# Kernel tuning notes

Measured on AMD Instinct MI355X. Metric: run time of the kernel, lower is better.

Reference implementation:

```python
import jax, jax.numpy as jnp
import numpy as np

N = 40000          # spots (nodes)
G = 3000           # genes (input features)
C = 20             # num_classes
E = N * 16         # edges (avg degree 16)


def _uniform(key, shape, stdv):
    return jax.random.uniform(key, shape, jnp.float32, -stdv, stdv)


def _linear_params(key, n_in, n_out):
    # torch Linear default init: U(-1/sqrt(in), 1/sqrt(in)); stored as [in, out]
    k1, k2 = jax.random.split(key)
    s = 1.0 / np.sqrt(n_in)
    return _uniform(k1, (n_in, n_out), s), _uniform(k2, (n_out,), s)


def setup_inputs() -> dict:
    key = jax.random.key(0)
    ks = jax.random.split(key, 32)
    x = jax.random.normal(ks[0], (N, G), jnp.float32)
    adj_rows = jax.random.randint(ks[1], (E,), 0, N, jnp.int32)
    adj_cols = jax.random.randint(ks[2], (E,), 0, N, jnp.int32)
    adj_vals = jax.random.uniform(ks[3], (E,), jnp.float32)

    # GCN weights: GraphConvolution init U(-1/sqrt(out), 1/sqrt(out)), no bias
    def gcn_w(k, fi, fo):
        return _uniform(k, (fi, fo), 1.0 / np.sqrt(fo))

    inp = {
        "x": x, "adj_rows": adj_rows, "adj_cols": adj_cols, "adj_vals": adj_vals,
        "W1": gcn_w(ks[4], G, 512), "W2": gcn_w(ks[5], 512, 256),
        "W3": gcn_w(ks[6], 256, 128), "W4": gcn_w(ks[7], 128, 128),
        "W5": gcn_w(ks[8], 128, C),
    }
    # AE linear layers
    for name, (fi, fo), k in [
        ("enc1", (G, 512), ks[9]), ("enc2", (512, 256), ks[10]),
        ("enc3", (256, 128), ks[11]), ("zl", (128, 128), ks[12]),
        ("dec1", (128, 128), ks[13]), ("dec2", (128, 256), ks[14]),
        ("dec3", (256, 512), ks[15]), ("xbar", (512, G), ks[16]),
    ]:
        w, b = _linear_params(k, fi, fo)
        inp[name + "_w"], inp[name + "_b"] = w, b
    # Attention projection vectors (Linear(in_size, 1, bias=False))
    inp["a1"] = _uniform(ks[17], (512,), 1.0 / np.sqrt(512))
    inp["a2"] = _uniform(ks[18], (256,), 1.0 / np.sqrt(256))
    inp["a3"] = _uniform(ks[19], (128,), 1.0 / np.sqrt(128))
    inp["a4"] = _uniform(ks[20], (128,), 1.0 / np.sqrt(128))
    inp["scale"] = jax.random.normal(ks[21], (G,), jnp.float32)
    inp["additive"] = jax.random.normal(ks[22], (G,), jnp.float32)
    return inp


def _spmm(rows, cols, vals, dense, n):
    # out[r] = sum_e vals[e] * dense[cols[e]] for rows[e]==r  (sparse [n,n] @ dense)
    return jax.ops.segment_sum(vals[:, None] * dense[cols], rows, num_segments=n)


def _gcn(x, rows, cols, vals, W, n, active=True):
    out = _spmm(rows, cols, vals, x @ W, n)
    return jax.nn.relu(out) if active else out


def _attn(h, t, a):
    # stack two [N,D] branches, softmax over the branch axis, weighted sum
    z = jnp.stack([h, t], axis=1)           # [N,2,D]
    w = jnp.einsum('nbd,d->nb', z, a)        # [N,2]
    beta = jax.nn.softmax(w, axis=1)
    return jnp.einsum('nb,nbd->nd', beta, z)


def reference(x, adj_rows, adj_cols, adj_vals,
              W1, W2, W3, W4, W5,
              enc1_w, enc1_b, enc2_w, enc2_b, enc3_w, enc3_b, zl_w, zl_b,
              dec1_w, dec1_b, dec2_w, dec2_b, dec3_w, dec3_b, xbar_w, xbar_b,
              a1, a2, a3, a4, scale, additive):
    n = x.shape[0]
    # autoencoder
    t1 = jax.nn.relu(x @ enc1_w + enc1_b)
    t2 = jax.nn.relu(t1 @ enc2_w + enc2_b)
    t3 = jax.nn.relu(t2 @ enc3_w + enc3_b)
    z = t3 @ zl_w + zl_b
    d1 = jax.nn.relu(z @ dec1_w + dec1_b)
    d2 = jax.nn.relu(d1 @ dec2_w + dec2_b)
    d3 = jax.nn.relu(d2 @ dec3_w + dec3_b)
    x_bar = d3 @ xbar_w + xbar_b
    # GCN stack with attention-fused AE skip connections
    h = _gcn(x, adj_rows, adj_cols, adj_vals, W1, n)
    emb = _attn(h, t1, a1)
    h = _gcn(emb, adj_rows, adj_cols, adj_vals, W2, n)
    emb = _attn(h, t2, a2)
    h = _gcn(emb, adj_rows, adj_cols, adj_vals, W3, n)
    emb = _attn(h, t3, a3)
    h = _gcn(emb, adj_rows, adj_cols, adj_vals, W4, n)
    emb = _attn(h, z, a4)
    output = _gcn(emb, adj_rows, adj_cols, adj_vals, W5, n, active=False)
    return output, x_bar, jax.nn.sigmoid(scale), jnp.exp(additive)
```

## Files before the change

### kernel.cpp

```cpp
#include <hip/hip_runtime.h>
#include <cmath>

typedef unsigned short u16;
typedef unsigned int u32;
typedef __attribute__((ext_vector_type(8))) short short8;
typedef __attribute__((ext_vector_type(4))) short short4v;
typedef __attribute__((ext_vector_type(4))) float f32x4;

__device__ __forceinline__ float bf2f(u16 h) {
  union { u32 u; float f; } v; v.u = ((u32)h) << 16; return v.f;
}
__device__ __forceinline__ u16 f2bf(float f) {
  union { float f; u32 u; } v; v.f = f;
  u32 u = v.u;
  u32 r = (u + 0x7FFFu + ((u >> 16) & 1u)) >> 16;
  return (u16)r;
}

__global__ void convx_kernel(const float* __restrict__ x, u16* __restrict__ A0) {
  int idx = blockIdx.x * 256 + threadIdx.x;
  int r = blockIdx.y;
  if (idx >= 752) return;
  short4v o;
  if (r < 40000 && idx < 750) {
    float4 v = *(const float4*)(x + (size_t)r * 3000 + idx * 4);
    o[0] = (short)f2bf(v.x); o[1] = (short)f2bf(v.y);
    o[2] = (short)f2bf(v.z); o[3] = (short)f2bf(v.w);
  } else {
    o[0] = 0; o[1] = 0; o[2] = 0; o[3] = 0;
  }
  *(short4v*)(A0 + (size_t)r * 3008 + idx * 4) = o;
}

__global__ void convw_kernel(const float* __restrict__ W, u16* __restrict__ Wt,
                             int K, int N, int Kp) {
  int k = blockIdx.x * 256 + threadIdx.x;
  int n = blockIdx.y;
  if (k >= Kp) return;
  float v = (k < K && n < N) ? W[(size_t)k * N + n] : 0.f;
  Wt[(size_t)n * Kp + k] = f2bf(v);
}

__global__ void zero_kernel(int* p, int n) {
  int i = blockIdx.x * 256 + threadIdx.x;
  if (i < n) p[i] = 0;
}
__global__ void count_kernel(const int* __restrict__ rows, int* __restrict__ counts, int E) {
  int i = blockIdx.x * 256 + threadIdx.x;
  if (i < E) atomicAdd(&counts[rows[i]], 1);
}
__global__ __launch_bounds__(1024) void scan_kernel(const int* __restrict__ counts,
                                                    int* __restrict__ rowptr,
                                                    int* __restrict__ cursor, int n) {
  __shared__ int buf[1024];
  __shared__ int carry_s;
  int tid = threadIdx.x;
  if (tid == 0) carry_s = 0;
  __syncthreads();
  for (int base = 0; base < n; base += 1024) {
    int i = base + tid;
    int v = (i < n) ? counts[i] : 0;
    buf[tid] = v;
    __syncthreads();
    for (int off = 1; off < 1024; off <<= 1) {
      int tv = (tid >= off) ? buf[tid - off] : 0;
      __syncthreads();
      buf[tid] += tv;
      __syncthreads();
    }
    int incl = buf[tid];
    int carry = carry_s;
    if (i < n) { int ex = carry + incl - v; rowptr[i] = ex; cursor[i] = ex; }
    __syncthreads();
    if (tid == 1023) carry_s = carry + incl;
    __syncthreads();
  }
  if (tid == 0) rowptr[n] = carry_s;
}
__global__ void scatter_kernel(const int* __restrict__ rows, const int* __restrict__ cols,
                               const float* __restrict__ vals, int* __restrict__ cursor,
                               int* __restrict__ cols_s, float* __restrict__ vals_s, int E) {
  int i = blockIdx.x * 256 + threadIdx.x;
  if (i < E) {
    int r = rows[i];
    int p = atomicAdd(&cursor[r], 1);
    cols_s[p] = cols[i];
    vals_s[p] = vals[i];
  }
}

#define BM 128
#define BN 128
#define BK 32

template <bool BIAS, bool RELU, bool OUTBF16, int CH>
__global__ __launch_bounds__(256, 2) void gemm_bf16(
    const u16* __restrict__ A, int lda, const u16* __restrict__ Bt, int ldb,
    void* __restrict__ C1, int ldc,
    const float* __restrict__ bias, int M, int Nreal, int K, int MT, int NT) {
  __shared__ __align__(16) u16 As[2][BM * BK];
  __shared__ __align__(16) u16 Bs[2][BN * BK];
  const int lin = blockIdx.x;
  const int per = CH * NT;
  const int g = lin / per;
  const int r0 = lin - g * per;
  const int bx0 = g * CH;
  const int cw = min(CH, MT - bx0);
  const int bx = bx0 + r0 % cw;
  const int by = r0 / cw;

  const int tid = threadIdx.x;
  const int lane = tid & 63;
  const int wave = tid >> 6;
  const int mblk = bx * BM;
  const int nblk = by * BN;
  const int wm = (wave & 1) * 64;
  const int wn = (wave >> 1) * 64;
  const int ml = lane & 15;
  const int kg = lane >> 4;

  f32x4 acc[4][4];
#pragma unroll
  for (int i = 0; i < 4; ++i)
#pragma unroll
    for (int j = 0; j < 4; ++j) acc[i][j] = (f32x4)(0.f);

  const int nk = K / BK;
  const int sr = tid >> 2;
  const int sc = (tid & 3) * 8;
  const u16* gA0 = A + (size_t)(mblk + sr) * lda + sc;
  const u16* gA1 = A + (size_t)(mblk + sr + 64) * lda + sc;
  const u16* gB0 = Bt + (size_t)(nblk + sr) * ldb + sc;
  const u16* gB1 = Bt + (size_t)(nblk + sr + 64) * ldb + sc;

  auto stage = [&](int buf, int kt) {
    const int ko = kt * BK;
    u16* lA = &As[buf][0] + wave * 512;
    u16* lB = &Bs[buf][0] + wave * 512;
    __builtin_amdgcn_global_load_lds((const void*)(gA0 + ko), (void*)lA, 16, 0, 0);
    __builtin_amdgcn_global_load_lds((const void*)(gA1 + ko), (void*)(lA + 2048), 16, 0, 0);
    __builtin_amdgcn_global_load_lds((const void*)(gB0 + ko), (void*)lB, 16, 0, 0);
    __builtin_amdgcn_global_load_lds((const void*)(gB1 + ko), (void*)(lB + 2048), 16, 0, 0);
  };

  stage(0, 0);
  asm volatile("s_waitcnt vmcnt(0)" ::: "memory");
  __syncthreads();

  int cur = 0;
  for (int kt = 0; kt < nk; ++kt) {
    if (kt + 1 < nk) stage(cur ^ 1, kt + 1);
    short8 af[4], bfr[4];
#pragma unroll
    for (int i = 0; i < 4; ++i) {
      af[i] = *(const short8*)&As[cur][(wm + i * 16 + ml) * BK + kg * 8];
      bfr[i] = *(const short8*)&Bs[cur][(wn + i * 16 + ml) * BK + kg * 8];
    }
#pragma unroll
    for (int i = 0; i < 4; ++i)
#pragma unroll
      for (int j = 0; j < 4; ++j)
        acc[i][j] = __builtin_amdgcn_mfma_f32_16x16x32_bf16(af[i], bfr[j], acc[i][j], 0, 0, 0);
    asm volatile("s_waitcnt vmcnt(0)" ::: "memory");
    __syncthreads();
    cur ^= 1;
  }

#pragma unroll
  for (int i = 0; i < 4; ++i) {
    const int row0 = mblk + wm + i * 16 + kg * 4;
#pragma unroll
    for (int j = 0; j < 4; ++j) {
      const int col = nblk + wn + j * 16 + ml;
      if (col < Nreal) {
        float bv = BIAS ? bias[col] : 0.f;
#pragma unroll
        for (int r = 0; r < 4; ++r) {
          const int row = row0 + r;
          if (row < M) {
            float v = acc[i][j][r] + bv;
            if (RELU) v = fmaxf(v, 0.f);
            if (OUTBF16)
              ((u16*)C1)[(size_t)row * ldc + col] = f2bf(v);
            else
              ((float*)C1)[(size_t)row * ldc + col] = v;
          }
        }
      }
    }
  }
}

template <bool BIAS, bool RELU, bool OUTBF16, bool SPLIT>
__global__ __launch_bounds__(512, 1) void gemm256(
    const u16* __restrict__ A, int lda, const u16* __restrict__ Bt, int ldb,
    void* __restrict__ C1, void* __restrict__ C2, int ldc,
    const float* __restrict__ bias, int M, int Nreal, int K, int MT2, int NT) {
  __shared__ __align__(16) u16 lds[2][2][256 * 64];
  const int tid = threadIdx.x;
  const int lane = tid & 63;
  const int wave = tid >> 6;
  const int wm = wave >> 2;
  const int wn = wave & 3;
  const int ml = lane & 15;
  const int kg = lane >> 4;

  const int grp = blockIdx.x / (8 * NT);
  const int rr = blockIdx.x % (8 * NT);
  const int nb = min(8, MT2 - grp * 8);
  const int bx = grp * 8 + rr % nb;
  const int by = rr / nb;
  const int mblk = bx * 256;
  const int nblk = by * 256;

  f32x4 acc[8][4];
#pragma unroll
  for (int i = 0; i < 8; ++i)
#pragma unroll
    for (int j = 0; j < 4; ++j) acc[i][j] = (f32x4)(0.f);

  const int srow = tid >> 3;
  const int clog = (tid & 7) ^ (srow & 7);
  const size_t abase = (size_t)(mblk + srow) * lda + clog * 8;
  const size_t bbase = (size_t)(nblk + srow) * ldb + clog * 8;
  const int NKT = K / 64;

  auto stageA = [&](int d, int kt, int h) {
    u16* dst = &lds[d][0][0] + h * 4096 + wave * 512;
    const u16* src = A + abase + (size_t)h * 64 * lda + kt * 64;
    __builtin_amdgcn_global_load_lds((const void*)src, (void*)dst, 16, 0, 0);
  };
  auto stageB = [&](int d, int kt, int h) {
    u16* dst = &lds[d][1][0] + h * 4096 + wave * 512;
    const u16* src = Bt + bbase + (size_t)h * 64 * ldb + kt * 64;
    __builtin_amdgcn_global_load_lds((const void*)src, (void*)dst, 16, 0, 0);
  };
  auto stageAll = [&](int d, int kt) {
    stageB(d, kt, 0); stageB(d, kt, 1); stageB(d, kt, 2); stageB(d, kt, 3);
    stageA(d, kt, 0); stageA(d, kt, 1); stageA(d, kt, 2); stageA(d, kt, 3);
  };
  auto readA = [&](int d, int im, int kk) -> short8 {
    const int r = wm * 128 + im * 16 + ml;
    const int ch = (kk * 4 + kg) ^ (r & 7);
    return *(const short8*)&lds[d][0][r * 64 + ch * 8];
  };
  auto readB = [&](int d, int j, int kk) -> short8 {
    const int r = wn * 64 + j * 16 + ml;
    const int ch = (kk * 4 + kg) ^ (r & 7);
    return *(const short8*)&lds[d][1][r * 64 + ch * 8];
  };

  stageAll(0, 0);
  __syncthreads();

  for (int kt = 0; kt < NKT; ++kt) {
    const int d = kt & 1;
    if (kt + 1 < NKT) stageAll(d ^ 1, kt + 1);

    short8 b[4][2];
#pragma unroll
    for (int j = 0; j < 4; ++j) { b[j][0] = readB(d, j, 0); b[j][1] = readB(d, j, 1); }
    short8 aC0k0 = readA(d, 0, 0), aC0k1 = readA(d, 0, 1);
    short8 aC1k0 = readA(d, 1, 0), aC1k1 = readA(d, 1, 1);
#pragma unroll
    for (int q = 0; q < 4; ++q) {
      short8 aN0k0, aN0k1, aN1k0, aN1k1;
      if (q < 3) {
        aN0k0 = readA(d, 2 * (q + 1), 0);     aN0k1 = readA(d, 2 * (q + 1), 1);
        aN1k0 = readA(d, 2 * (q + 1) + 1, 0); aN1k1 = readA(d, 2 * (q + 1) + 1, 1);
      }
      __builtin_amdgcn_s_setprio(1);
#pragma unroll
      for (int j = 0; j < 4; ++j) {
        acc[2 * q][j]     = __builtin_amdgcn_mfma_f32_16x16x32_bf16(aC0k0, b[j][0], acc[2 * q][j], 0, 0, 0);
        acc[2 * q + 1][j] = __builtin_amdgcn_mfma_f32_16x16x32_bf16(aC1k0, b[j][0], acc[2 * q + 1][j], 0, 0, 0);
      }
#pragma unroll
      for (int j = 0; j < 4; ++j) {
        acc[2 * q][j]     = __builtin_amdgcn_mfma_f32_16x16x32_bf16(aC0k1, b[j][1], acc[2 * q][j], 0, 0, 0);
        acc[2 * q + 1][j] = __builtin_amdgcn_mfma_f32_16x16x32_bf16(aC1k1, b[j][1], acc[2 * q + 1][j], 0, 0, 0);
      }
      __builtin_amdgcn_s_setprio(0);
      if (q < 3) { aC0k0 = aN0k0; aC0k1 = aN0k1; aC1k0 = aN1k0; aC1k1 = aN1k1; }
    }
    __syncthreads();
  }

  const int crow0 = mblk + wm * 128;
  const int ccol0 = nblk + wn * 64;
#pragma unroll
  for (int i = 0; i < 8; ++i) {
    const int row0 = crow0 + i * 16 + kg * 4;
#pragma unroll
    for (int j = 0; j < 4; ++j) {
      const int col = ccol0 + j * 16 + ml;
      if (SPLIT) {
        const bool second = (nblk >= 512);
        const float bv = second ? 0.f : bias[col];
#pragma unroll
        for (int r = 0; r < 4; ++r) {
          const int row = row0 + r;
          if (row < M) {
            float v = acc[i][j][r] + bv;
            if (!second) v = fmaxf(v, 0.f);
            u16* dst = second ? (u16*)C2 : (u16*)C1;
            dst[(size_t)row * 512 + (second ? col - 512 : col)] = f2bf(v);
          }
        }
      } else if (col < Nreal) {
        const float bv = BIAS ? bias[col] : 0.f;
#pragma unroll
        for (int r = 0; r < 4; ++r) {
          const int row = row0 + r;
          if (row < M) {
            float v = acc[i][j][r] + bv;
            if (RELU) v = fmaxf(v, 0.f);
            if (OUTBF16)
              ((u16*)C1)[(size_t)row * ldc + col] = f2bf(v);
            else
              ((float*)C1)[(size_t)row * ldc + col] = v;
          }
        }
      }
    }
  }
}

template <int D, bool RELU>
__global__ __launch_bounds__(256) void spmm_vec(const int* __restrict__ rowptr,
                                                const int* __restrict__ colidx,
                                                const float* __restrict__ vals,
                                                const u16* __restrict__ X,
                                                u16* __restrict__ Y) {
  constexpr int VE = D / 64;
  const int wave = threadIdx.x >> 6, lane = threadIdx.x & 63;
  const int row = blockIdx.x * 4 + wave;
  const int co = lane * VE;
  float acc[VE];
#pragma unroll
  for (int j = 0; j < VE; ++j) acc[j] = 0.f;
  const int s = rowptr[row], e = rowptr[row + 1];
  for (int i = s; i < e; ++i) {
    const int c = colidx[i];
    const float v = vals[i];
    const u16* xr = X + (size_t)c * D + co;
    if constexpr (VE == 8) {
      short8 x8 = *(const short8*)xr;
#pragma unroll
      for (int j = 0; j < 8; ++j) acc[j] += v * bf2f((u16)x8[j]);
    } else if constexpr (VE == 4) {
      short4v x4 = *(const short4v*)xr;
#pragma unroll
      for (int j = 0; j < 4; ++j) acc[j] += v * bf2f((u16)x4[j]);
    } else {
      u32 x2 = *(const u32*)xr;
      acc[0] += v * bf2f((u16)(x2 & 0xffffu));
      acc[1] += v * bf2f((u16)(x2 >> 16));
    }
  }
  u16* yr = Y + (size_t)row * D + co;
  if constexpr (VE == 8) {
    short8 o;
#pragma unroll
    for (int j = 0; j < 8; ++j) { float f = RELU ? fmaxf(acc[j], 0.f) : acc[j]; o[j] = (short)f2bf(f); }
    *(short8*)yr = o;
  } else if constexpr (VE == 4) {
    short4v o;
#pragma unroll
    for (int j = 0; j < 4; ++j) { float f = RELU ? fmaxf(acc[j], 0.f) : acc[j]; o[j] = (short)f2bf(f); }
    *(short4v*)yr = o;
  } else {
    float f0 = RELU ? fmaxf(acc[0], 0.f) : acc[0];
    float f1 = RELU ? fmaxf(acc[1], 0.f) : acc[1];
    *(u32*)yr = (u32)f2bf(f0) | ((u32)f2bf(f1) << 16);
  }
}

__global__ __launch_bounds__(64) void spmm_out_kernel(const int* __restrict__ rowptr,
                                                      const int* __restrict__ colidx,
                                                      const float* __restrict__ vals,
                                                      const u16* __restrict__ X,
                                                      float* __restrict__ Y) {
  int row = blockIdx.x;
  int c = threadIdx.x;
  float acc = 0.f;
  int s = rowptr[row], e = rowptr[row + 1];
  for (int i = s; i < e; ++i) {
    int col = colidx[i];
    float v = vals[i];
    if (c < 20) acc += v * bf2f(X[(size_t)col * 20 + c]);
  }
  if (c < 20) Y[(size_t)row * 20 + c] = acc;
}

template <int D>
__global__ __launch_bounds__(256) void attn_vec(const u16* __restrict__ h,
                                                const u16* __restrict__ t,
                                                const float* __restrict__ a,
                                                u16* __restrict__ emb) {
  constexpr int VE = D / 64;
  const int wave = threadIdx.x >> 6, lane = threadIdx.x & 63;
  const int row = blockIdx.x * 4 + wave;
  const int co = lane * VE;
  const u16* hr = h + (size_t)row * D + co;
  const u16* tr = t + (size_t)row * D + co;
  float hv[VE], tv[VE];
  if constexpr (VE == 8) {
    short8 h8 = *(const short8*)hr, t8 = *(const short8*)tr;
#pragma unroll
    for (int j = 0; j < 8; ++j) { hv[j] = bf2f((u16)h8[j]); tv[j] = bf2f((u16)t8[j]); }
  } else if constexpr (VE == 4) {
    short4v h4 = *(const short4v*)hr, t4 = *(const short4v*)tr;
#pragma unroll
    for (int j = 0; j < 4; ++j) { hv[j] = bf2f((u16)h4[j]); tv[j] = bf2f((u16)t4[j]); }
  } else {
    u32 h2 = *(const u32*)hr, t2 = *(const u32*)tr;
    hv[0] = bf2f((u16)(h2 & 0xffffu)); hv[1] = bf2f((u16)(h2 >> 16));
    tv[0] = bf2f((u16)(t2 & 0xffffu)); tv[1] = bf2f((u16)(t2 >> 16));
  }
  float wh = 0.f, wt = 0.f;
#pragma unroll
  for (int j = 0; j < VE; ++j) {
    float av = a[co + j];
    wh += av * hv[j];
    wt += av * tv[j];
  }
  for (int off = 32; off; off >>= 1) {
    wh += __shfl_xor(wh, off);
    wt += __shfl_xor(wt, off);
  }
  float m = fmaxf(wh, wt);
  float e1 = expf(wh - m), e2 = expf(wt - m);
  float inv = 1.f / (e1 + e2);
  float b1 = e1 * inv, b2 = e2 * inv;
  u16* er = emb + (size_t)row * D + co;
  if constexpr (VE == 8) {
    short8 o;
#pragma unroll
    for (int j = 0; j < 8; ++j) o[j] = (short)f2bf(b1 * hv[j] + b2 * tv[j]);
    *(short8*)er = o;
  } else if constexpr (VE == 4) {
    short4v o;
#pragma unroll
    for (int j = 0; j < 4; ++j) o[j] = (short)f2bf(b1 * hv[j] + b2 * tv[j]);
    *(short4v*)er = o;
  } else {
    *(u32*)er = (u32)f2bf(b1 * hv[0] + b2 * tv[0]) | ((u32)f2bf(b1 * hv[1] + b2 * tv[1]) << 16);
  }
}

__global__ __launch_bounds__(64) void xw5_kernel(const u16* __restrict__ emb,
                                                 const float* __restrict__ W5,
                                                 u16* __restrict__ xw5) {
  int row = blockIdx.x;
  int c = threadIdx.x;
  if (c >= 20) return;
  const short8* er = (const short8*)(emb + (size_t)row * 128);
  float acc = 0.f;
#pragma unroll
  for (int k8 = 0; k8 < 16; ++k8) {
    short8 v = er[k8];
#pragma unroll
    for (int j = 0; j < 8; ++j) acc += bf2f((u16)v[j]) * W5[(k8 * 8 + j) * 20 + c];
  }
  xw5[(size_t)row * 20 + c] = f2bf(acc);
}

__global__ void sig_exp_kernel(const float* __restrict__ scale, const float* __restrict__ additive,
                               float* __restrict__ osig, float* __restrict__ oexp, int g) {
  int i = blockIdx.x * 256 + threadIdx.x;
  if (i < g) {
    osig[i] = 1.f / (1.f + expf(-scale[i]));
    oexp[i] = expf(additive[i]);
  }
}

extern "C" void kernel_launch(void* const* d_in, const int* in_sizes, int n_in,
                              void* d_out, int out_size, void* d_ws, size_t ws_size,
                              hipStream_t stream) {
  (void)n_in; (void)out_size; (void)ws_size;
  const float* x      = (const float*)d_in[0];
  const int*   arows  = (const int*)d_in[1];
  const int*   acols  = (const int*)d_in[2];
  const float* avals  = (const float*)d_in[3];
  const float* W1     = (const float*)d_in[4];
  const float* W2     = (const float*)d_in[5];
  const float* W3     = (const float*)d_in[6];
  const float* W4     = (const float*)d_in[7];
  const float* W5     = (const float*)d_in[8];
  const float* enc1_w = (const float*)d_in[9],  *enc1_b = (const float*)d_in[10];
  const float* enc2_w = (const float*)d_in[11], *enc2_b = (const float*)d_in[12];
  const float* enc3_w = (const float*)d_in[13], *enc3_b = (const float*)d_in[14];
  const float* zl_w   = (const float*)d_in[15], *zl_b   = (const float*)d_in[16];
  const float* dec1_w = (const float*)d_in[17], *dec1_b = (const float*)d_in[18];
  const float* dec2_w = (const float*)d_in[19], *dec2_b = (const float*)d_in[20];
  const float* dec3_w = (const float*)d_in[21], *dec3_b = (const float*)d_in[22];
  const float* xbar_w = (const float*)d_in[23], *xbar_b = (const float*)d_in[24];
  const float* a1 = (const float*)d_in[25], *a2 = (const float*)d_in[26];
  const float* a3 = (const float*)d_in[27], *a4 = (const float*)d_in[28];
  const float* scale = (const float*)d_in[29], *additive = (const float*)d_in[30];

  const int E = in_sizes[1];
  const int N = 40000, G = 3000, Kx = 3008;
  const int Mp = 40192;

  float* out      = (float*)d_out;
  float* out_gcn  = out;
  float* out_xbar = out + (size_t)N * 20;
  float* out_sig  = out_xbar + (size_t)N * G;
  float* out_exp  = out_sig + G;

  char* wsb = (char*)d_ws;
  size_t off = 0;
  auto alloc = [&](size_t b) -> void* {
    void* p = wsb + off;
    off = (off + b + 255) & ~(size_t)255;
    return p;
  };
  u16* A0    = (u16*)alloc((size_t)Mp * Kx * 2);
  u16* t1    = (u16*)alloc((size_t)Mp * 512 * 2);
  u16* t2    = (u16*)alloc((size_t)Mp * 256 * 2);
  u16* t3    = (u16*)alloc((size_t)Mp * 128 * 2);
  u16* zb    = (u16*)alloc((size_t)Mp * 128 * 2);
  u16* dd1   = (u16*)alloc((size_t)Mp * 128 * 2);
  u16* dd2   = (u16*)alloc((size_t)Mp * 256 * 2);
  u16* dd3   = (u16*)alloc((size_t)Mp * 512 * 2);
  u16* xw    = (u16*)alloc((size_t)Mp * 512 * 2);
  u16* hb    = (u16*)alloc((size_t)Mp * 512 * 2);
  u16* emb   = (u16*)alloc((size_t)Mp * 512 * 2);
  u16* xw5   = (u16*)alloc((size_t)N * 20 * 2);
  u16* catT  = (u16*)alloc((size_t)1024 * Kx * 2);
  u16* enc2T = (u16*)alloc((size_t)256 * 512 * 2);
  u16* enc3T = (u16*)alloc((size_t)128 * 256 * 2);
  u16* zlT   = (u16*)alloc((size_t)128 * 128 * 2);
  u16* dec1T = (u16*)alloc((size_t)128 * 128 * 2);
  u16* dec2T = (u16*)alloc((size_t)256 * 128 * 2);
  u16* dec3T = (u16*)alloc((size_t)512 * 256 * 2);
  u16* xbarT = (u16*)alloc((size_t)3072 * 512 * 2);
  u16* W2T   = (u16*)alloc((size_t)256 * 512 * 2);
  u16* W3T   = (u16*)alloc((size_t)128 * 256 * 2);
  u16* W4T   = (u16*)alloc((size_t)128 * 128 * 2);
  int* counts = (int*)alloc((size_t)N * 4);
  int* rowptr = (int*)alloc((size_t)(N + 1) * 4);
  int* cursor = (int*)alloc((size_t)N * 4);
  int* colss  = (int*)alloc((size_t)E * 4);
  float* valss = (float*)alloc((size_t)E * 4);

  convx_kernel<<<dim3(3, Mp), 256, 0, stream>>>(x, A0);
  auto convw = [&](const float* W, u16* Wt, int K, int Nw, int Kp, int Np) {
    convw_kernel<<<dim3((Kp + 255) / 256, Np), 256, 0, stream>>>(W, Wt, K, Nw, Kp);
  };
  convw(enc1_w, catT,             3000, 512, Kx, 512);
  convw(W1,     catT + 512 * Kx,  3000, 512, Kx, 512);
  convw(enc2_w, enc2T, 512, 256, 512, 256);
  convw(enc3_w, enc3T, 256, 128, 256, 128);
  convw(zl_w,   zlT,   128, 128, 128, 128);
  convw(dec1_w, dec1T, 128, 128, 128, 128);
  convw(dec2_w, dec2T, 128, 256, 128, 256);
  convw(dec3_w, dec3T, 256, 512, 256, 512);
  convw(xbar_w, xbarT, 512, 3000, 512, 3072);
  convw(W2,     W2T,   512, 256, 512, 256);
  convw(W3,     W3T,   256, 128, 256, 128);
  convw(W4,     W4T,   128, 128, 128, 128);

  zero_kernel<<<(N + 255) / 256, 256, 0, stream>>>(counts, N);
  count_kernel<<<(E + 255) / 256, 256, 0, stream>>>(arows, counts, E);
  scan_kernel<<<1, 1024, 0, stream>>>(counts, rowptr, cursor, N);
  scatter_kernel<<<(E + 255) / 256, 256, 0, stream>>>(arows, acols, avals, cursor, colss, valss, E);

  const int MT = 313;
  const int MT2 = 157;
  gemm256<false, false, true, true><<<MT2 * 4, 512, 0, stream>>>(
      A0, Kx, catT, Kx, t1, xw, 512, enc1_b, N, 1024, Kx, MT2, 4);
  gemm_bf16<true, true, true, 32><<<MT * 2, 256, 0, stream>>>(
      t1, 512, enc2T, 512, t2, 256, enc2_b, N, 256, 512, MT, 2);
  gemm_bf16<true, true, true, 32><<<MT * 1, 256, 0, stream>>>(
      t2, 256, enc3T, 256, t3, 128, enc3_b, N, 128, 256, MT, 1);
  gemm_bf16<true, false, true, 32><<<MT * 1, 256, 0, stream>>>(
      t3, 128, zlT, 128, zb, 128, zl_b, N, 128, 128, MT, 1);
  gemm_bf16<true, true, true, 32><<<MT * 1, 256, 0, stream>>>(
      zb, 128, dec1T, 128, dd1, 128, dec1_b, N, 128, 128, MT, 1);
  gemm_bf16<true, true, true, 32><<<MT * 2, 256, 0, stream>>>(
      dd1, 128, dec2T, 128, dd2, 256, dec2_b, N, 256, 128, MT, 2);
  gemm256<true, true, true, false><<<MT2 * 2, 512, 0, stream>>>(
      dd2, 256, dec3T, 256, dd3, nullptr, 512, dec3_b, N, 512, 256, MT2, 2);
  gemm256<true, false, false, false><<<MT2 * 12, 512, 0, stream>>>(
      dd3, 512, xbarT, 512, out_xbar, nullptr, 3000, xbar_b, N, 3000, 512, MT2, 12);

  spmm_vec<512, true><<<N / 4, 256, 0, stream>>>(rowptr, colss, valss, xw, hb);
  attn_vec<512><<<N / 4, 256, 0, stream>>>(hb, t1, a1, emb);
  gemm_bf16<false, false, true, 32><<<MT * 2, 256, 0, stream>>>(
      emb, 512, W2T, 512, xw, 256, nullptr, N, 256, 512, MT, 2);
  spmm_vec<256, true><<<N / 4, 256, 0, stream>>>(rowptr, colss, valss, xw, hb);
  attn_vec<256><<<N / 4, 256, 0, stream>>>(hb, t2, a2, emb);
  gemm_bf16<false, false, true, 32><<<MT * 1, 256, 0, stream>>>(
      emb, 256, W3T, 256, xw, 128, nullptr, N, 128, 256, MT, 1);
  spmm_vec<128, true><<<N / 4, 256, 0, stream>>>(rowptr, colss, valss, xw, hb);
  attn_vec<128><<<N / 4, 256, 0, stream>>>(hb, t3, a3, emb);
  gemm_bf16<false, false, true, 32><<<MT * 1, 256, 0, stream>>>(
      emb, 128, W4T, 128, xw, 128, nullptr, N, 128, 128, MT, 1);
  spmm_vec<128, true><<<N / 4, 256, 0, stream>>>(rowptr, colss, valss, xw, hb);
  attn_vec<128><<<N / 4, 256, 0, stream>>>(hb, zb, a4, emb);

  xw5_kernel<<<N, 64, 0, stream>>>(emb, W5, xw5);
  spmm_out_kernel<<<N, 64, 0, stream>>>(rowptr, colss, valss, xw5, out_gcn);

  sig_exp_kernel<<<(G + 255) / 256, 256, 0, stream>>>(scale, additive, out_sig, out_exp, G);
}
```

Measured before the change: 1.472 ms.

## Fuse SpMM with attention and shrink big GEMM tiles to 128x256

Merges each SpMM with the attention combine that follows it, so the aggregated features stay in registers and the hb intermediate is never written or read back from global memory. The large GEMM kernel now uses 128-row M tiles instead of 256, which doubles the grid and cuts per-block LDS and accumulator registers. The dec3 GEMM moves from the 256-tile kernel to the smaller gemm_bf16 kernel. Smaller tiles raise occupancy and improve load balance over the CUs, but they lower per-block reuse of the B operand.

```diff
diff --git a/kernel.cpp b/kernel.cpp
--- a/kernel.cpp
+++ b/kernel.cpp
@@ -192,11 +192,12 @@
 }
 
 template <bool BIAS, bool RELU, bool OUTBF16, bool SPLIT>
-__global__ __launch_bounds__(512, 1) void gemm256(
+__global__ __launch_bounds__(512, 1) void gemm256v2(
     const u16* __restrict__ A, int lda, const u16* __restrict__ Bt, int ldb,
     void* __restrict__ C1, void* __restrict__ C2, int ldc,
-    const float* __restrict__ bias, int M, int Nreal, int K, int MT2, int NT) {
-  __shared__ __align__(16) u16 lds[2][2][256 * 64];
+    const float* __restrict__ bias, int M, int Nreal, int K, int MT, int NT) {
+  __shared__ __align__(16) u16 As[2][128 * 64];
+  __shared__ __align__(16) u16 Bs[2][256 * 64];
   const int tid = threadIdx.x;
   const int lane = tid & 63;
   const int wave = tid >> 6;
@@ -207,15 +208,15 @@
 
   const int grp = blockIdx.x / (8 * NT);
   const int rr = blockIdx.x % (8 * NT);
-  const int nb = min(8, MT2 - grp * 8);
+  const int nb = min(8, MT - grp * 8);
   const int bx = grp * 8 + rr % nb;
   const int by = rr / nb;
-  const int mblk = bx * 256;
+  const int mblk = bx * 128;
   const int nblk = by * 256;
 
-  f32x4 acc[8][4];
-#pragma unroll
-  for (int i = 0; i < 8; ++i)
+  f32x4 acc[4][4];
+#pragma unroll
+  for (int i = 0; i < 4; ++i)
 #pragma unroll
     for (int j = 0; j < 4; ++j) acc[i][j] = (f32x4)(0.f);
 
@@ -226,28 +227,28 @@
   const int NKT = K / 64;
 
   auto stageA = [&](int d, int kt, int h) {
-    u16* dst = &lds[d][0][0] + h * 4096 + wave * 512;
+    u16* dst = &As[d][0] + h * 4096 + wave * 512;
     const u16* src = A + abase + (size_t)h * 64 * lda + kt * 64;
     __builtin_amdgcn_global_load_lds((const void*)src, (void*)dst, 16, 0, 0);
   };
   auto stageB = [&](int d, int kt, int h) {
-    u16* dst = &lds[d][1][0] + h * 4096 + wave * 512;
+    u16* dst = &Bs[d][0] + h * 4096 + wave * 512;
     const u16* src = Bt + bbase + (size_t)h * 64 * ldb + kt * 64;
     __builtin_amdgcn_global_load_lds((const void*)src, (void*)dst, 16, 0, 0);
   };
   auto stageAll = [&](int d, int kt) {
     stageB(d, kt, 0); stageB(d, kt, 1); stageB(d, kt, 2); stageB(d, kt, 3);
-    stageA(d, kt, 0); stageA(d, kt, 1); stageA(d, kt, 2); stageA(d, kt, 3);
+    stageA(d, kt, 0); stageA(d, kt, 1);
   };
   auto readA = [&](int d, int im, int kk) -> short8 {
-    const int r = wm * 128 + im * 16 + ml;
+    const int r = wm * 64 + im * 16 + ml;
     const int ch = (kk * 4 + kg) ^ (r & 7);
-    return *(const short8*)&lds[d][0][r * 64 + ch * 8];
+    return *(const short8*)&As[d][r * 64 + ch * 8];
   };
   auto readB = [&](int d, int j, int kk) -> short8 {
     const int r = wn * 64 + j * 16 + ml;
     const int ch = (kk * 4 + kg) ^ (r & 7);
-    return *(const short8*)&lds[d][1][r * 64 + ch * 8];
+    return *(const short8*)&Bs[d][r * 64 + ch * 8];
   };
 
   stageAll(0, 0);
@@ -263,11 +264,11 @@
     short8 aC0k0 = readA(d, 0, 0), aC0k1 = readA(d, 0, 1);
     short8 aC1k0 = readA(d, 1, 0), aC1k1 = readA(d, 1, 1);
 #pragma unroll
-    for (int q = 0; q < 4; ++q) {
+    for (int q = 0; q < 2; ++q) {
       short8 aN0k0, aN0k1, aN1k0, aN1k1;
-      if (q < 3) {
-        aN0k0 = readA(d, 2 * (q + 1), 0);     aN0k1 = readA(d, 2 * (q + 1), 1);
-        aN1k0 = readA(d, 2 * (q + 1) + 1, 0); aN1k1 = readA(d, 2 * (q + 1) + 1, 1);
+      if (q == 0) {
+        aN0k0 = readA(d, 2, 0); aN0k1 = readA(d, 2, 1);
+        aN1k0 = readA(d, 3, 0); aN1k1 = readA(d, 3, 1);
       }
       __builtin_amdgcn_s_setprio(1);
 #pragma unroll
@@ -281,15 +282,15 @@
         acc[2 * q + 1][j] = __builtin_amdgcn_mfma_f32_16x16x32_bf16(aC1k1, b[j][1], acc[2 * q + 1][j], 0, 0, 0);
       }
       __builtin_amdgcn_s_setprio(0);
-      if (q < 3) { aC0k0 = aN0k0; aC0k1 = aN0k1; aC1k0 = aN1k0; aC1k1 = aN1k1; }
+      if (q == 0) { aC0k0 = aN0k0; aC0k1 = aN0k1; aC1k0 = aN1k0; aC1k1 = aN1k1; }
     }
     __syncthreads();
   }
 
-  const int crow0 = mblk + wm * 128;
+  const int crow0 = mblk + wm * 64;
   const int ccol0 = nblk + wn * 64;
 #pragma unroll
-  for (int i = 0; i < 8; ++i) {
+  for (int i = 0; i < 4; ++i) {
     const int row0 = crow0 + i * 16 + kg * 4;
 #pragma unroll
     for (int j = 0; j < 4; ++j) {
@@ -326,19 +327,21 @@
   }
 }
 
-template <int D, bool RELU>
-__global__ __launch_bounds__(256) void spmm_vec(const int* __restrict__ rowptr,
-                                                const int* __restrict__ colidx,
-                                                const float* __restrict__ vals,
-                                                const u16* __restrict__ X,
-                                                u16* __restrict__ Y) {
+template <int D>
+__global__ __launch_bounds__(256) void spmm_attn(const int* __restrict__ rowptr,
+                                                 const int* __restrict__ colidx,
+                                                 const float* __restrict__ vals,
+                                                 const u16* __restrict__ X,
+                                                 const u16* __restrict__ T,
+                                                 const float* __restrict__ a,
+                                                 u16* __restrict__ emb) {
   constexpr int VE = D / 64;
   const int wave = threadIdx.x >> 6, lane = threadIdx.x & 63;
   const int row = blockIdx.x * 4 + wave;
   const int co = lane * VE;
-  float acc[VE];
-#pragma unroll
-  for (int j = 0; j < VE; ++j) acc[j] = 0.f;
+  float h[VE];
+#pragma unroll
+  for (int j = 0; j < VE; ++j) h[j] = 0.f;
   const int s = rowptr[row], e = rowptr[row + 1];
   for (int i = s; i < e; ++i) {
     const int c = colidx[i];
@@ -347,32 +350,63 @@
     if constexpr (VE == 8) {
       short8 x8 = *(const short8*)xr;
 #pragma unroll
-      for (int j = 0; j < 8; ++j) acc[j] += v * bf2f((u16)x8[j]);
+      for (int j = 0; j < 8; ++j) h[j] += v * bf2f((u16)x8[j]);
     } else if constexpr (VE == 4) {
       short4v x4 = *(const short4v*)xr;
 #pragma unroll
-      for (int j = 0; j < 4; ++j) acc[j] += v * bf2f((u16)x4[j]);
+      for (int j = 0; j < 4; ++j) h[j] += v * bf2f((u16)x4[j]);
     } else {
       u32 x2 = *(const u32*)xr;
-      acc[0] += v * bf2f((u16)(x2 & 0xffffu));
-      acc[1] += v * bf2f((u16)(x2 >> 16));
+      h[0] += v * bf2f((u16)(x2 & 0xffffu));
+      h[1] += v * bf2f((u16)(x2 >> 16));
     }
   }
-  u16* yr = Y + (size_t)row * D + co;
+#pragma unroll
+  for (int j = 0; j < VE; ++j) h[j] = fmaxf(h[j], 0.f);
+
+  float tv[VE];
+  const u16* tr = T + (size_t)row * D + co;
+  if constexpr (VE == 8) {
+    short8 t8 = *(const short8*)tr;
+#pragma unroll
+    for (int j = 0; j < 8; ++j) tv[j] = bf2f((u16)t8[j]);
+  } else if constexpr (VE == 4) {
+    short4v t4 = *(const short4v*)tr;
+#pragma unroll
+    for (int j = 0; j < 4; ++j) tv[j] = bf2f((u16)t4[j]);
+  } else {
+    u32 t2 = *(const u32*)tr;
+    tv[0] = bf2f((u16)(t2 & 0xffffu)); tv[1] = bf2f((u16)(t2 >> 16));
+  }
+
+  float wh = 0.f, wt = 0.f;
+#pragma unroll
+  for (int j = 0; j < VE; ++j) {
+    float av = a[co + j];
+    wh += av * h[j];
+    wt += av * tv[j];
+  }
+  for (int off = 32; off; off >>= 1) {
+    wh += __shfl_xor(wh, off);
+    wt += __shfl_xor(wt, off);
+  }
+  float m = fmaxf(wh, wt);
+  float e1 = expf(wh - m), e2 = expf(wt - m);
+  float inv = 1.f / (e1 + e2);
+  float b1 = e1 * inv, b2 = e2 * inv;
+  u16* er = emb + (size_t)row * D + co;
   if constexpr (VE == 8) {
     short8 o;
 #pragma unroll
-    for (int j = 0; j < 8; ++j) { float f = RELU ? fmaxf(acc[j], 0.f) : acc[j]; o[j] = (short)f2bf(f); }
-    *(short8*)yr = o;
+    for (int j = 0; j < 8; ++j) o[j] = (short)f2bf(b1 * h[j] + b2 * tv[j]);
+    *(short8*)er = o;
   } else if constexpr (VE == 4) {
     short4v o;
 #pragma unroll
-    for (int j = 0; j < 4; ++j) { float f = RELU ? fmaxf(acc[j], 0.f) : acc[j]; o[j] = (short)f2bf(f); }
-    *(short4v*)yr = o;
+    for (int j = 0; j < 4; ++j) o[j] = (short)f2bf(b1 * h[j] + b2 * tv[j]);
+    *(short4v*)er = o;
   } else {
-    float f0 = RELU ? fmaxf(acc[0], 0.f) : acc[0];
-    float f1 = RELU ? fmaxf(acc[1], 0.f) : acc[1];
-    *(u32*)yr = (u32)f2bf(f0) | ((u32)f2bf(f1) << 16);
+    *(u32*)er = (u32)f2bf(b1 * h[0] + b2 * tv[0]) | ((u32)f2bf(b1 * h[1] + b2 * tv[1]) << 16);
   }
 }
 
@@ -391,62 +425,6 @@
     if (c < 20) acc += v * bf2f(X[(size_t)col * 20 + c]);
   }
   if (c < 20) Y[(size_t)row * 20 + c] = acc;
-}
-
-template <int D>
-__global__ __launch_bounds__(256) void attn_vec(const u16* __restrict__ h,
-                                                const u16* __restrict__ t,
-                                                const float* __restrict__ a,
-                                                u16* __restrict__ emb) {
-  constexpr int VE = D / 64;
-  const int wave = threadIdx.x >> 6, lane = threadIdx.x & 63;
-  const int row = blockIdx.x * 4 + wave;
-  const int co = lane * VE;
-  const u16* hr = h + (size_t)row * D + co;
-  const u16* tr = t + (size_t)row * D + co;
-  float hv[VE], tv[VE];
-  if constexpr (VE == 8) {
-    short8 h8 = *(const short8*)hr, t8 = *(const short8*)tr;
-#pragma unroll
-    for (int j = 0; j < 8; ++j) { hv[j] = bf2f((u16)h8[j]); tv[j] = bf2f((u16)t8[j]); }
-  } else if constexpr (VE == 4) {
-    short4v h4 = *(const short4v*)hr, t4 = *(const short4v*)tr;
-#pragma unroll
-    for (int j = 0; j < 4; ++j) { hv[j] = bf2f((u16)h4[j]); tv[j] = bf2f((u16)t4[j]); }
-  } else {
-    u32 h2 = *(const u32*)hr, t2 = *(const u32*)tr;
-    hv[0] = bf2f((u16)(h2 & 0xffffu)); hv[1] = bf2f((u16)(h2 >> 16));
-    tv[0] = bf2f((u16)(t2 & 0xffffu)); tv[1] = bf2f((u16)(t2 >> 16));
-  }
-  float wh = 0.f, wt = 0.f;
-#pragma unroll
-  for (int j = 0; j < VE; ++j) {
-    float av = a[co + j];
-    wh += av * hv[j];
-    wt += av * tv[j];
-  }
-  for (int off = 32; off; off >>= 1) {
-    wh += __shfl_xor(wh, off);
-    wt += __shfl_xor(wt, off);
-  }
-  float m = fmaxf(wh, wt);
-  float e1 = expf(wh - m), e2 = expf(wt - m);
-  float inv = 1.f / (e1 + e2);
-  float b1 = e1 * inv, b2 = e2 * inv;
-  u16* er = emb + (size_t)row * D + co;
-  if constexpr (VE == 8) {
-    short8 o;
-#pragma unroll
-    for (int j = 0; j < 8; ++j) o[j] = (short)f2bf(b1 * hv[j] + b2 * tv[j]);
-    *(short8*)er = o;
-  } else if constexpr (VE == 4) {
-    short4v o;
-#pragma unroll
-    for (int j = 0; j < 4; ++j) o[j] = (short)f2bf(b1 * hv[j] + b2 * tv[j]);
-    *(short4v*)er = o;
-  } else {
-    *(u32*)er = (u32)f2bf(b1 * hv[0] + b2 * tv[0]) | ((u32)f2bf(b1 * hv[1] + b2 * tv[1]) << 16);
-  }
 }
 
 __global__ __launch_bounds__(64) void xw5_kernel(const u16* __restrict__ emb,
@@ -526,7 +504,6 @@
   u16* dd2   = (u16*)alloc((size_t)Mp * 256 * 2);
   u16* dd3   = (u16*)alloc((size_t)Mp * 512 * 2);
   u16* xw    = (u16*)alloc((size_t)Mp * 512 * 2);
-  u16* hb    = (u16*)alloc((size_t)Mp * 512 * 2);
   u16* emb   = (u16*)alloc((size_t)Mp * 512 * 2);
   u16* xw5   = (u16*)alloc((size_t)N * 20 * 2);
   u16* catT  = (u16*)alloc((size_t)1024 * Kx * 2);
@@ -569,9 +546,8 @@
   scatter_kernel<<<(E + 255) / 256, 256, 0, stream>>>(arows, acols, avals, cursor, colss, valss, E);
 
   const int MT = 313;
-  const int MT2 = 157;
-  gemm256<false, false, true, true><<<MT2 * 4, 512, 0, stream>>>(
-      A0, Kx, catT, Kx, t1, xw, 512, enc1_b, N, 1024, Kx, MT2, 4);
+  gemm256v2<false, false, true, true><<<MT * 4, 512, 0, stream>>>(
+      A0, Kx, catT, Kx, t1, xw, 512, enc1_b, N, 1024, Kx, MT, 4);
   gemm_bf16<true, true, true, 32><<<MT * 2, 256, 0, stream>>>(
       t1, 512, enc2T, 512, t2, 256, enc2_b, N, 256, 512, MT, 2);
   gemm_bf16<true, true, true, 32><<<MT * 1, 256, 0, stream>>>(
@@ -582,25 +558,21 @@
       zb, 128, dec1T, 128, dd1, 128, dec1_b, N, 128, 128, MT, 1);
   gemm_bf16<true, true, true, 32><<<MT * 2, 256, 0, stream>>>(
       dd1, 128, dec2T, 128, dd2, 256, dec2_b, N, 256, 128, MT, 2);
-  gemm256<true, true, true, false><<<MT2 * 2, 512, 0, stream>>>(
-      dd2, 256, dec3T, 256, dd3, nullptr, 512, dec3_b, N, 512, 256, MT2, 2);
-  gemm256<true, false, false, false><<<MT2 * 12, 512, 0, stream>>>(
-      dd3, 512, xbarT, 512, out_xbar, nullptr, 3000, xbar_b, N, 3000, 512, MT2, 12);
-
-  spmm_vec<512, true><<<N / 4, 256, 0, stream>>>(rowptr, colss, valss, xw, hb);
-  attn_vec<512><<<N / 4, 256, 0, stream>>>(hb, t1, a1, emb);
+  gemm_bf16<true, true, true, 32><<<MT * 4, 256, 0, stream>>>(
+      dd2, 256, dec3T, 256, dd3, 512, dec3_b, N, 512, 256, MT, 4);
+  gemm256v2<true, false, false, false><<<MT * 12, 512, 0, stream>>>(
+      dd3, 512, xbarT, 512, out_xbar, nullptr, 3000, xbar_b, N, 3000, 512, MT, 12);
+
+  spmm_attn<512><<<N / 4, 256, 0, stream>>>(rowptr, colss, valss, xw, t1, a1, emb);
   gemm_bf16<false, false, true, 32><<<MT * 2, 256, 0, stream>>>(
       emb, 512, W2T, 512, xw, 256, nullptr, N, 256, 512, MT, 2);
-  spmm_vec<256, true><<<N / 4, 256, 0, stream>>>(rowptr, colss, valss, xw, hb);
-  attn_vec<256><<<N / 4, 256, 0, stream>>>(hb, t2, a2, emb);
+  spmm_attn<256><<<N / 4, 256, 0, stream>>>(rowptr, colss, valss, xw, t2, a2, emb);
   gemm_bf16<false, false, true, 32><<<MT * 1, 256, 0, stream>>>(
       emb, 256, W3T, 256, xw, 128, nullptr, N, 128, 256, MT, 1);
-  spmm_vec<128, true><<<N / 4, 256, 0, stream>>>(rowptr, colss, valss, xw, hb);
-  attn_vec<128><<<N / 4, 256, 0, stream>>>(hb, t3, a3, emb);
+  spmm_attn<128><<<N / 4, 256, 0, stream>>>(rowptr, colss, valss, xw, t3, a3, emb);
   gemm_bf16<false, false, true, 32><<<MT * 1, 256, 0, stream>>>(
       emb, 128, W4T, 128, xw, 128, nullptr, N, 128, 128, MT, 1);
-  spmm_vec<128, true><<<N / 4, 256, 0, stream>>>(rowptr, colss, valss, xw, hb);
-  attn_vec<128><<<N / 4, 256, 0, stream>>>(hb, zb, a4, emb);
+  spmm_attn<128><<<N / 4, 256, 0, stream>>>(rowptr, colss, valss, xw, zb, a4, emb);
 
   xw5_kernel<<<N, 64, 0, stream>>>(emb, W5, xw5);
   spmm_out_kernel<<<N, 64, 0, stream>>>(rowptr, colss, valss, xw5, out_gcn);
```

Result: slower. 1.528 ms (+3.8%).
